# Optimization experiments

Measured on AMD Instinct MI355X. Metric: run time of the kernel, lower is better.

Reference implementation:

```python
import jax, jax.numpy as jnp
import numpy as np

TEMPERATURE = 1.0
B, D = 8192, 256


def setup_inputs() -> dict:
    key = jax.random.key(0)
    k1, k2 = jax.random.split(key)
    return {
        "encoder_embedding1": jax.random.normal(k1, (B, D), dtype=jnp.float32),
        "encoder_embedding2": jax.random.normal(k2, (B, D), dtype=jnp.float32),
    }


def _l2_normalize(x, eps=1e-8):
    # matches torch CosineSimilarity eps handling closely enough for fp32
    n = jnp.sqrt(jnp.sum(x * x, axis=-1, keepdims=True))
    return x / jnp.maximum(n, eps)


def reference(encoder_embedding1, encoder_embedding2):
    # sim[i, j] = cos(contrast_i, anchor_j); torch builds this via a (B,B,D)
    # expand + elementwise CosineSimilarity — here it's a normalized matmul.
    a = _l2_normalize(encoder_embedding1)  # anchors  [B, D]
    c = _l2_normalize(encoder_embedding2)  # contrast [B, D]
    sim = jnp.einsum("id,jd->ij", c, a)    # [B, B]
    log_probs = jax.nn.log_softmax(sim / TEMPERATURE, axis=0)
    loss = -jnp.sum(jnp.diagonal(log_probs)) * TEMPERATURE
    return loss
```

## Files before the change

### kernel.cpp

```cpp
#include <hip/hip_runtime.h>
#include <hip/hip_bf16.h>
#include <hip/hip_fp8.h>


#define BROWS 8192
#define DIM   256

typedef int   i32x4 __attribute__((ext_vector_type(4)));
typedef int   i32x8 __attribute__((ext_vector_type(8)));
typedef float f32x4 __attribute__((ext_vector_type(4)));

__device__ __forceinline__ void gload_lds16(const void* g, void* l) {
  __builtin_amdgcn_global_load_lds(
      (const __attribute__((address_space(1))) unsigned int*)g,
      (__attribute__((address_space(3))) unsigned int*)l, 16, 0, 0);
}

__device__ __forceinline__ unsigned char to_e4m3(float v) {
  __hip_fp8_e4m3 t(v);
  return *reinterpret_cast<unsigned char*>(&t);
}

__global__ __launch_bounds__(256) void prep_kernel(
    const float* __restrict__ E1, const float* __restrict__ E2,
    unsigned char* __restrict__ An8, unsigned char* __restrict__ Cn8,
    float* __restrict__ diag, float* __restrict__ colsum) {
  if (blockIdx.x < 32) colsum[blockIdx.x * 256 + threadIdx.x] = 0.f;

  const int w    = threadIdx.x >> 6;
  const int lane = threadIdx.x & 63;
  const int row  = blockIdx.x * 4 + w;
  const size_t base = (size_t)row * DIM + lane * 4;

  const float4 a = *(const float4*)(E1 + base);
  const float4 c = *(const float4*)(E2 + base);

  float sa  = a.x*a.x + a.y*a.y + a.z*a.z + a.w*a.w;
  float sc  = c.x*c.x + c.y*c.y + c.z*c.z + c.w*c.w;
  float sac = a.x*c.x + a.y*c.y + a.z*c.z + a.w*c.w;
#pragma unroll
  for (int o = 32; o > 0; o >>= 1) {
    sa  += __shfl_down(sa,  o);
    sc  += __shfl_down(sc,  o);
    sac += __shfl_down(sac, o);
  }
  const float inva = 1.0f / fmaxf(sqrtf(__shfl(sa, 0)), 1e-8f);
  const float invc = 1.0f / fmaxf(sqrtf(__shfl(sc, 0)), 1e-8f);

  uchar4 pa, pc;
  pa.x = to_e4m3(a.x * inva); pa.y = to_e4m3(a.y * inva);
  pa.z = to_e4m3(a.z * inva); pa.w = to_e4m3(a.w * inva);
  pc.x = to_e4m3(c.x * invc); pc.y = to_e4m3(c.y * invc);
  pc.z = to_e4m3(c.z * invc); pc.w = to_e4m3(c.w * invc);
  *(uchar4*)(An8 + base) = pa;
  *(uchar4*)(Cn8 + base) = pc;
  if (lane == 0) diag[row] = sac * inva * invc;
}

__global__ __launch_bounds__(256, 2) void gemm_colsum_kernel(
    const unsigned char* __restrict__ Cn8,
    const unsigned char* __restrict__ An8,
    float* __restrict__ colsum) {
  __shared__ __align__(16) unsigned char ldsC[32768];
  __shared__ __align__(16) unsigned char ldsA[2][16384];

  const int tid  = threadIdx.x;
  const int lane = tid & 63;
  const int w    = tid >> 6;
  const int wr   = w >> 1;
  const int wc   = w & 1;

  const int jgroup = blockIdx.x & 15;
  const int itile  = blockIdx.x >> 4;
  const int i0 = itile * 128;
  const int j0 = jgroup * 512;

  const int sr = tid >> 4;
  const int pl = (tid & 15) ^ (sr & 7);
  const unsigned char* gC = Cn8 + (size_t)(i0 + sr) * DIM + pl * 16;
  const unsigned char* gA = An8 + (size_t)(j0 + sr) * DIM + pl * 16;

  auto stageA = [&](int jj, int buf) {
#pragma unroll
    for (int r = 0; r < 4; ++r)
      gload_lds16(gA + (size_t)(jj * 64 + r * 16) * DIM,
                  &ldsA[buf][0] + r * 4096 + w * 1024);
  };

#pragma unroll
  for (int r = 0; r < 8; ++r)
    gload_lds16(gC + (size_t)(r * 16) * DIM, &ldsC[0] + r * 4096 + w * 1024);
  stageA(0, 0);
  stageA(1, 1);

  asm volatile("s_waitcnt vmcnt(8)" ::: "memory");
  __builtin_amdgcn_sched_barrier(0);
  __builtin_amdgcn_s_barrier();

  const int q  = lane >> 4;
  const int rb = lane & 15;
  const int SC = 0x7F7F7F7F;

  i32x8 af[4][2];
#pragma unroll
  for (int m = 0; m < 4; ++m) {
    const int r = wr * 64 + m * 16 + rb;
#pragma unroll
    for (int W = 0; W < 2; ++W) {
      const int s0 = (W * 8 + q * 2)     ^ (r & 7);
      const int s1 = (W * 8 + q * 2 + 1) ^ (r & 7);
      union { i32x4 h[2]; i32x8 v; } u;
      u.h[0] = *(const i32x4*)(&ldsC[0] + r * 256 + s0 * 16);
      u.h[1] = *(const i32x4*)(&ldsC[0] + r * 256 + s1 * 16);
      af[m][W] = u.v;
    }
  }
  asm volatile("s_waitcnt lgkmcnt(0)" ::: "memory");
  __builtin_amdgcn_sched_barrier(0);

#pragma unroll
  for (int jj = 0; jj < 8; ++jj) {
    const int b = jj & 1;
    if (jj == 0)      asm volatile("s_waitcnt vmcnt(4)" ::: "memory");
    else if (jj == 1) asm volatile("s_waitcnt vmcnt(6)" ::: "memory");
    else if (jj == 7) asm volatile("s_waitcnt vmcnt(4)" ::: "memory");
    else              asm volatile("s_waitcnt vmcnt(8)" ::: "memory");
    __builtin_amdgcn_sched_barrier(0);
    __builtin_amdgcn_s_barrier();

    i32x8 bf[2][2];
#pragma unroll
    for (int n = 0; n < 2; ++n) {
      const int r = wc * 32 + n * 16 + rb;
#pragma unroll
      for (int W = 0; W < 2; ++W) {
        const int s0 = (W * 8 + q * 2)     ^ (r & 7);
        const int s1 = (W * 8 + q * 2 + 1) ^ (r & 7);
        union { i32x4 h[2]; i32x8 v; } u;
        u.h[0] = *(const i32x4*)(&ldsA[b][0] + r * 256 + s0 * 16);
        u.h[1] = *(const i32x4*)(&ldsA[b][0] + r * 256 + s1 * 16);
        bf[n][W] = u.v;
      }
    }
    asm volatile("s_waitcnt lgkmcnt(0)" ::: "memory");
    __builtin_amdgcn_sched_barrier(0);
    __builtin_amdgcn_s_barrier();
    __builtin_amdgcn_sched_barrier(0);

    if (jj < 6) stageA(jj + 2, b);
    __builtin_amdgcn_sched_barrier(0);

    f32x4 acc[4][2] = {};
    __builtin_amdgcn_s_setprio(1);
#pragma unroll
    for (int m = 0; m < 4; ++m)
#pragma unroll
      for (int n = 0; n < 2; ++n)
#pragma unroll
        for (int W = 0; W < 2; ++W)
          acc[m][n] = __builtin_amdgcn_mfma_scale_f32_16x16x128_f8f6f4(
              af[m][W], bf[n][W], acc[m][n], 0, 0, 0, SC, 0, SC);
    __builtin_amdgcn_s_setprio(0);
    __builtin_amdgcn_sched_barrier(0);

#pragma unroll
    for (int n = 0; n < 2; ++n) {
      float s = 0.f;
#pragma unroll
      for (int m = 0; m < 4; ++m) {
        const f32x4 v = acc[m][n];
        s += __expf(v[0]) + __expf(v[1]) + __expf(v[2]) + __expf(v[3]);
      }
      s += __shfl_xor(s, 16);
      s += __shfl_xor(s, 32);
      if (lane < 16)
        atomicAdd(&colsum[j0 + jj * 64 + wc * 32 + n * 16 + lane], s);
    }
    __builtin_amdgcn_sched_barrier(0);
  }
}

__global__ __launch_bounds__(256) void finalize_kernel(
    const float* __restrict__ colsum, const float* __restrict__ diag,
    float* __restrict__ out) {
  const int t = threadIdx.x;
  float s = 0.f;
  for (int j = t; j < BROWS; j += 256) s += logf(colsum[j]) - diag[j];
#pragma unroll
  for (int o = 32; o > 0; o >>= 1) s += __shfl_down(s, o);
  __shared__ float red[4];
  if ((t & 63) == 0) red[t >> 6] = s;
  __syncthreads();
  if (t == 0) out[0] = red[0] + red[1] + red[2] + red[3];
}

extern "C" void kernel_launch(void* const* d_in, const int* in_sizes, int n_in,
                              void* d_out, int out_size, void* d_ws, size_t ws_size,
                              hipStream_t stream) {
  const float* E1 = (const float*)d_in[0];
  const float* E2 = (const float*)d_in[1];
  char* ws = (char*)d_ws;
  unsigned char* Cn8 = (unsigned char*)(ws);
  unsigned char* An8 = (unsigned char*)(ws + (size_t)2 * 1024 * 1024);
  float* colsum = (float*)(ws + (size_t)4 * 1024 * 1024);
  float* diag   = (float*)(ws + (size_t)4 * 1024 * 1024 + 32 * 1024);
  float* out = (float*)d_out;

  prep_kernel<<<BROWS / 4, 256, 0, stream>>>(E1, E2, An8, Cn8, diag, colsum);
  gemm_colsum_kernel<<<64 * 16, 256, 0, stream>>>(Cn8, An8, colsum);
  finalize_kernel<<<1, 256, 0, stream>>>(colsum, diag, out);
}
```

Measured before the change: 46.27 us.

## Reuse LDS for A tiles after C fragments load, fuse finalize via last-block counter

The GEMM kernel now loads the C tile into a single 32KB LDS buffer, reads it into registers, then reuses the same buffer for the double-buffered A tiles. This halves LDS use per block so occupancy can rise from 2 to 3 blocks per CU. The separate finalize launch is removed: a global atomic counter lets the last finishing block compute the log-sum reduction. In exchange, the A prefetch can no longer overlap the C load, and register pressure tightens under the higher occupancy bound.

```diff
diff --git a/kernel.cpp b/kernel.cpp
--- a/kernel.cpp
+++ b/kernel.cpp
@@ -24,8 +24,10 @@
 __global__ __launch_bounds__(256) void prep_kernel(
     const float* __restrict__ E1, const float* __restrict__ E2,
     unsigned char* __restrict__ An8, unsigned char* __restrict__ Cn8,
-    float* __restrict__ diag, float* __restrict__ colsum) {
+    float* __restrict__ diag, float* __restrict__ colsum,
+    unsigned int* __restrict__ counter) {
   if (blockIdx.x < 32) colsum[blockIdx.x * 256 + threadIdx.x] = 0.f;
+  if (blockIdx.x == 0 && threadIdx.x == 0) counter[0] = 0u;
 
   const int w    = threadIdx.x >> 6;
   const int lane = threadIdx.x & 63;
@@ -57,12 +59,14 @@
   if (lane == 0) diag[row] = sac * inva * invc;
 }
 
-__global__ __launch_bounds__(256, 2) void gemm_colsum_kernel(
+__global__ __launch_bounds__(256, 3) void gemm_colsum_kernel(
     const unsigned char* __restrict__ Cn8,
     const unsigned char* __restrict__ An8,
-    float* __restrict__ colsum) {
-  __shared__ __align__(16) unsigned char ldsC[32768];
-  __shared__ __align__(16) unsigned char ldsA[2][16384];
+    float* __restrict__ colsum, const float* __restrict__ diag,
+    float* __restrict__ out, unsigned int* __restrict__ counter) {
+  __shared__ __align__(16) unsigned char lds[32768];
+  __shared__ unsigned int isLast;
+  __shared__ float red[4];
 
   const int tid  = threadIdx.x;
   const int lane = tid & 63;
@@ -80,20 +84,10 @@
   const unsigned char* gC = Cn8 + (size_t)(i0 + sr) * DIM + pl * 16;
   const unsigned char* gA = An8 + (size_t)(j0 + sr) * DIM + pl * 16;
 
-  auto stageA = [&](int jj, int buf) {
-#pragma unroll
-    for (int r = 0; r < 4; ++r)
-      gload_lds16(gA + (size_t)(jj * 64 + r * 16) * DIM,
-                  &ldsA[buf][0] + r * 4096 + w * 1024);
-  };
-
 #pragma unroll
   for (int r = 0; r < 8; ++r)
-    gload_lds16(gC + (size_t)(r * 16) * DIM, &ldsC[0] + r * 4096 + w * 1024);
-  stageA(0, 0);
-  stageA(1, 1);
-
-  asm volatile("s_waitcnt vmcnt(8)" ::: "memory");
+    gload_lds16(gC + (size_t)(r * 16) * DIM, &lds[0] + r * 4096 + w * 1024);
+  asm volatile("s_waitcnt vmcnt(0)" ::: "memory");
   __builtin_amdgcn_sched_barrier(0);
   __builtin_amdgcn_s_barrier();
 
@@ -110,13 +104,24 @@
       const int s0 = (W * 8 + q * 2)     ^ (r & 7);
       const int s1 = (W * 8 + q * 2 + 1) ^ (r & 7);
       union { i32x4 h[2]; i32x8 v; } u;
-      u.h[0] = *(const i32x4*)(&ldsC[0] + r * 256 + s0 * 16);
-      u.h[1] = *(const i32x4*)(&ldsC[0] + r * 256 + s1 * 16);
+      u.h[0] = *(const i32x4*)(&lds[0] + r * 256 + s0 * 16);
+      u.h[1] = *(const i32x4*)(&lds[0] + r * 256 + s1 * 16);
       af[m][W] = u.v;
     }
   }
   asm volatile("s_waitcnt lgkmcnt(0)" ::: "memory");
   __builtin_amdgcn_sched_barrier(0);
+  __builtin_amdgcn_s_barrier();
+  __builtin_amdgcn_sched_barrier(0);
+
+  auto stageA = [&](int jj, int buf) {
+#pragma unroll
+    for (int r = 0; r < 4; ++r)
+      gload_lds16(gA + (size_t)(jj * 64 + r * 16) * DIM,
+                  &lds[0] + buf * 16384 + r * 4096 + w * 1024);
+  };
+  stageA(0, 0);
+  stageA(1, 1);
 
 #pragma unroll
   for (int jj = 0; jj < 8; ++jj) {
@@ -137,8 +142,8 @@
         const int s0 = (W * 8 + q * 2)     ^ (r & 7);
         const int s1 = (W * 8 + q * 2 + 1) ^ (r & 7);
         union { i32x4 h[2]; i32x8 v; } u;
-        u.h[0] = *(const i32x4*)(&ldsA[b][0] + r * 256 + s0 * 16);
-        u.h[1] = *(const i32x4*)(&ldsA[b][0] + r * 256 + s1 * 16);
+        u.h[0] = *(const i32x4*)(&lds[0] + b * 16384 + r * 256 + s0 * 16);
+        u.h[1] = *(const i32x4*)(&lds[0] + b * 16384 + r * 256 + s1 * 16);
         bf[n][W] = u.v;
       }
     }
@@ -178,20 +183,22 @@
     }
     __builtin_amdgcn_sched_barrier(0);
   }
-}
-
-__global__ __launch_bounds__(256) void finalize_kernel(
-    const float* __restrict__ colsum, const float* __restrict__ diag,
-    float* __restrict__ out) {
-  const int t = threadIdx.x;
-  float s = 0.f;
-  for (int j = t; j < BROWS; j += 256) s += logf(colsum[j]) - diag[j];
-#pragma unroll
-  for (int o = 32; o > 0; o >>= 1) s += __shfl_down(s, o);
-  __shared__ float red[4];
-  if ((t & 63) == 0) red[t >> 6] = s;
+
+  __threadfence();
   __syncthreads();
-  if (t == 0) out[0] = red[0] + red[1] + red[2] + red[3];
+  if (tid == 0) isLast = (atomicAdd(counter, 1u) == (unsigned)(gridDim.x - 1));
+  __syncthreads();
+  if (isLast) {
+    __threadfence();
+    volatile const float* cs = colsum;
+    float s = 0.f;
+    for (int j = tid; j < BROWS; j += 256) s += logf(cs[j]) - diag[j];
+#pragma unroll
+    for (int o = 32; o > 0; o >>= 1) s += __shfl_down(s, o);
+    if ((tid & 63) == 0) red[tid >> 6] = s;
+    __syncthreads();
+    if (tid == 0) out[0] = red[0] + red[1] + red[2] + red[3];
+  }
 }
 
 extern "C" void kernel_launch(void* const* d_in, const int* in_sizes, int n_in,
@@ -204,9 +211,9 @@
   unsigned char* An8 = (unsigned char*)(ws + (size_t)2 * 1024 * 1024);
   float* colsum = (float*)(ws + (size_t)4 * 1024 * 1024);
   float* diag   = (float*)(ws + (size_t)4 * 1024 * 1024 + 32 * 1024);
+  unsigned int* counter = (unsigned int*)(ws + (size_t)4 * 1024 * 1024 + 64 * 1024);
   float* out = (float*)d_out;
 
-  prep_kernel<<<BROWS / 4, 256, 0, stream>>>(E1, E2, An8, Cn8, diag, colsum);
-  gemm_colsum_kernel<<<64 * 16, 256, 0, stream>>>(Cn8, An8, colsum);
-  finalize_kernel<<<1, 256, 0, stream>>>(colsum, diag, out);
-}
+  prep_kernel<<<BROWS / 4, 256, 0, stream>>>(E1, E2, An8, Cn8, diag, colsum, counter);
+  gemm_colsum_kernel<<<64 * 16, 256, 0, stream>>>(Cn8, An8, colsum, diag, out, counter);
+}
```

After: 112.1 us. 142% more time.
